# Kernel optimization log

Hardware: AMD Instinct MI355X
Metric: run time of the kernel (lower is better)

## Reference

```python
import jax, jax.numpy as jnp
import numpy as np

H = W = 64          # spatial size
WH = WW = 8         # window size
C = 384             # embed dim
NH = 12             # heads
HD = C // NH        # head dim
SH, SW = WH // 2, WW // 2   # shift
N = WH * WW         # tokens per window
NW = (H // WH) * (W // WW)  # windows per image
SCALE = C ** -0.5   # NOTE: original scales by embed_dim**-0.5, not head_dim


def _to_windows(x, B):
    # (B, H*W, C) -> (B*NW, N, C)
    x = x.reshape(B, H // WH, WH, W // WW, WW, C)
    x = x.transpose(0, 1, 3, 2, 4, 5)
    return x.reshape(B * NW, N, C)


def _to_spatial(x, B):
    # (B*NW, N, C) -> (B, H*W, C)
    x = x.reshape(B, H // WH, W // WW, WH, WW, C)
    x = x.transpose(0, 1, 3, 2, 4, 5)
    return x.reshape(B, H * W, C)


def setup_inputs() -> dict:
    key = jax.random.key(0)
    ks = jax.random.split(key, 4)
    x = jax.random.normal(ks[0], (32, H * W, C), jnp.float32)
    w_qkv = jax.random.normal(ks[1], (C, 3 * C), jnp.float32) * (1.0 / np.sqrt(C))
    w_proj = jax.random.normal(ks[2], (C, C), jnp.float32) * (1.0 / np.sqrt(C))
    b_proj = jnp.zeros((C,), jnp.float32)
    emb_table = jax.random.normal(ks[3], (2 * (WH - 1) + 1 + 2 * (WW - 1) + 1, NH), jnp.float32) * 0.02

    # relative-position bias indices (create_bias_indices)
    hmax, wmax = WH - 1, WW - 1
    h_abs = np.repeat(np.arange(WH), WW)
    w_abs = np.tile(np.arange(WW), WH)
    h_rel = h_abs[None, :] - h_abs[:, None]
    w_rel = w_abs[None, :] - w_abs[:, None]
    h_idx = np.clip(h_rel, -hmax, hmax) + hmax                      # offset 0
    w_idx = np.clip(w_rel, -wmax, wmax) + wmax + (2 * hmax + 1)     # offset 2*hmax+1
    indices = jnp.asarray(np.stack([h_idx, w_idx]), jnp.int32)      # (2, N, N)

    # shift mask (create_shift_mask)
    id_map = np.zeros((H, W))
    h_slices = [(0, -WH), (-WH, -SH), (-SH, None)]
    w_slices = [(0, -WW), (-WW, -SW), (-SW, None)]
    cnt = 0
    for hs, he in h_slices:
        for ws, we in w_slices:
            id_map[hs:he, ws:we] = cnt
            cnt += 1
    idw = id_map.reshape(H // WH, WH, W // WW, WW).transpose(0, 2, 1, 3).reshape(NW, N)
    diff = idw[:, None, :] - idw[:, :, None]
    shift_mask = jnp.asarray(np.where(diff != 0, -1e9, 0.0), jnp.float32)  # (NW, N, N)

    return dict(x=x, w_qkv=w_qkv, w_proj=w_proj, b_proj=b_proj,
                emb_table=emb_table, indices=indices, shift_mask=shift_mask)


def reference(x, w_qkv, w_proj, b_proj, emb_table, indices, shift_mask):
    B = x.shape[0]
    # cyclic shift
    xg = x.reshape(B, H, W, C)
    xg = jnp.roll(xg, (-SH, -SW), axis=(1, 2)).reshape(B, H * W, C)
    xw = _to_windows(xg, B)                                   # (B*NW, N, C)
    qkv = xw @ w_qkv                                          # (B*NW, N, 3C)
    qkv = qkv.reshape(B * NW, N, 3, NH, HD).transpose(2, 0, 3, 1, 4)
    q, k, v = qkv[0] * SCALE, qkv[1], qkv[2]                  # (B*NW, NH, N, HD)
    s = jnp.einsum('bhnc,bhmc->bhnm', q, k)
    # relative-position bias: gather twice (h and w tables) and sum
    bias = emb_table[indices].sum(0).transpose(2, 0, 1)       # (NH, N, N)
    s = s + bias[None]
    # per-window-group additive shift mask
    s = s.reshape(B, NW, NH, N, N) + shift_mask[None, :, None]
    s = s.reshape(B * NW, NH, N, N)
    a = jax.nn.softmax(s, axis=-1)
    o = jnp.einsum('bhnm,bhmc->bhnc', a, v)
    o = o.transpose(0, 2, 1, 3).reshape(B * NW, N, C)
    o = o @ w_proj + b_proj
    o = _to_spatial(o, B)
    # reverse cyclic shift
    o = jnp.roll(o.reshape(B, H, W, C), (SH, SW), axis=(1, 2)).reshape(B, H * W, C)
    return o
```

## Files before the change

kernel.cpp:

```cpp
#include <hip/hip_runtime.h>
#include <hip/hip_bf16.h>

typedef __bf16 bf16x8 __attribute__((ext_vector_type(8)));
typedef float f32x4 __attribute__((ext_vector_type(4)));
typedef float f32x4v __attribute__((ext_vector_type(4)));
typedef unsigned short u16x8 __attribute__((ext_vector_type(8)));
typedef unsigned short u16x4 __attribute__((ext_vector_type(4)));

#define NHEADS 12
#define SCALE 0.05103103630798288f
#define MFMA __builtin_amdgcn_mfma_f32_16x16x32_bf16

static __device__ __forceinline__ unsigned short f2b(float f){
    unsigned u = __float_as_uint(f);
    unsigned r = u + 0x7FFFu + ((u >> 16) & 1u);
    return (unsigned short)(r >> 16);
}
static __device__ __forceinline__ float b2f(unsigned short u){
    union { float f; unsigned u32; } v; v.u32 = ((unsigned)u) << 16; return v.f;
}

__global__ void prep_full(const float* __restrict__ wqkv, const float* __restrict__ wproj,
                          const float* __restrict__ emb, const int* __restrict__ indices,
                          const float* __restrict__ mask,
                          unsigned short* __restrict__ wqkvP,
                          unsigned short* __restrict__ wprojP,
                          unsigned short* __restrict__ bm2){
    int i = blockIdx.x * 256 + threadIdx.x;
    if (i < 442368){
        int j = i & 7, rest = i >> 3;
        int ln = rest & 63; rest >>= 6;
        int kf = rest % 12, t = rest / 12;
        int k = kf * 32 + (ln >> 4) * 8 + j;
        int col = t * 16 + (ln & 15);
        wqkvP[i] = f2b(wqkv[k * 1152 + col]);
        return;
    }
    i -= 442368;
    if (i < 147456){
        int j = i & 7, rest = i >> 3;
        int ln = rest & 63; rest >>= 6;
        int kf = rest % 12, t = rest / 12;
        int k = kf * 32 + (ln >> 4) * 8 + j;
        int col = t * 16 + (ln & 15);
        wprojP[i] = f2b(wproj[k * 384 + col]);
        return;
    }
    i -= 147456;
    if (i < 64 * 12 * 4096){
        int w = i / 49152, rem = i % 49152;
        int h = rem / 4096, r2 = rem & 4095;
        int col = r2 >> 6, row = r2 & 63;
        int ij = row * 64 + col;
        float v = emb[indices[ij] * 12 + h] + emb[indices[4096 + ij] * 12 + h]
                + mask[w * 4096 + ij];
        bm2[i] = f2b(v);
    }
}

__global__ __launch_bounds__(256, 3) void qkv_gemm(
    const float* __restrict__ x, const unsigned short* __restrict__ wqkvP,
    unsigned short* __restrict__ qg, unsigned short* __restrict__ kg,
    unsigned short* __restrict__ vg)
{
    __shared__ unsigned short As[64 * 384];
    __shared__ unsigned short tbuf[4 * 512];
    const int tid = threadIdx.x, wave = tid >> 6, lane = tid & 63;
    const int lo = lane & 15, hi = lane >> 4;
    const int win = blockIdx.x;
    const int widx = win & 63, wh = widx >> 3, ww = widx & 7, b = win >> 6;

    {
        const int r = tid >> 2;
        const int ih = r >> 3, iw = r & 7;
        const int gh = (wh * 8 + ih + 4) & 63, gw = (ww * 8 + iw + 4) & 63;
        const float* src = x + ((size_t)(b * 4096 + gh * 64 + gw)) * 384;
        unsigned short* dst = As + r * 384;
        const int sw = r & 7;
        #pragma unroll
        for (int i = 0; i < 12; ++i){
            const int c = (tid & 3) + i * 4;
            f32x4v f0 = __builtin_nontemporal_load(
                reinterpret_cast<const f32x4v*>(src + c * 8));
            f32x4v f1 = __builtin_nontemporal_load(
                reinterpret_cast<const f32x4v*>(src + c * 8 + 4));
            union { bf16x8 v; unsigned short s[8]; } u;
            u.s[0]=f2b(f0[0]); u.s[1]=f2b(f0[1]); u.s[2]=f2b(f0[2]); u.s[3]=f2b(f0[3]);
            u.s[4]=f2b(f1[0]); u.s[5]=f2b(f1[1]); u.s[6]=f2b(f1[2]); u.s[7]=f2b(f1[3]);
            const int cs = (c & ~7) | ((c & 7) ^ sw);
            *reinterpret_cast<bf16x8*>(dst + cs * 8) = u.v;
        }
    }
    __syncthreads();

    #pragma unroll 1
    for (int nc = 0; nc < 9; ++nc){
        const int t0 = nc * 8 + wave * 2;
        const unsigned short* bp = wqkvP + (size_t)t0 * 12 * 512 + lane * 8;
        f32x4 acc[4][2];
        #pragma unroll
        for (int rt = 0; rt < 4; ++rt){ acc[rt][0] = {0,0,0,0}; acc[rt][1] = {0,0,0,0}; }
        #pragma unroll
        for (int kf = 0; kf < 12; ++kf){
            bf16x8 b0 = *reinterpret_cast<const bf16x8*>(bp + kf * 512);
            bf16x8 b1 = *reinterpret_cast<const bf16x8*>(bp + (12 + kf) * 512);
            const int c = kf * 4 + hi;
            #pragma unroll
            for (int rt = 0; rt < 4; ++rt){
                const int r = rt * 16 + lo;
                const int cs = (c & ~7) | ((c & 7) ^ (r & 7));
                bf16x8 af = *reinterpret_cast<const bf16x8*>(As + r * 384 + cs * 8);
                acc[rt][0] = MFMA(af, b0, acc[rt][0], 0, 0, 0);
                acc[rt][1] = MFMA(af, b1, acc[rt][1], 0, 0, 0);
            }
        }
        const int base = nc * 128 + wave * 32;
        const int m = base / 384;
        const int h = (base % 384) >> 5;
        const size_t pair = (size_t)(win * 12 + h);
        if (m == 2){
            #pragma unroll
            for (int ct = 0; ct < 2; ++ct){
                const int d = ct * 16 + lo;
                #pragma unroll
                for (int rt = 0; rt < 4; ++rt){
                    u16x4 u;
                    u[0] = f2b(acc[rt][ct][0]); u[1] = f2b(acc[rt][ct][1]);
                    u[2] = f2b(acc[rt][ct][2]); u[3] = f2b(acc[rt][ct][3]);
                    __builtin_nontemporal_store(u, reinterpret_cast<u16x4*>(
                        vg + pair * 2048 + (size_t)d * 64 + rt * 16 + hi * 4));
                }
            }
        } else {
            unsigned short* tb = tbuf + wave * 512;
            const float sc = (m == 0) ? SCALE : 1.0f;
            unsigned short* dstb = (m == 0 ? qg : kg) + pair * 2048;
            #pragma unroll
            for (int rt = 0; rt < 4; ++rt){
                asm volatile("" ::: "memory");
                #pragma unroll
                for (int ct = 0; ct < 2; ++ct)
                    #pragma unroll
                    for (int r4 = 0; r4 < 4; ++r4)
                        tb[(hi * 4 + r4) * 32 + ct * 16 + lo] = f2b(acc[rt][ct][r4] * sc);
                asm volatile("" ::: "memory");
                u16x8 v = *reinterpret_cast<const u16x8*>(
                    tb + (lane >> 2) * 32 + (lane & 3) * 8);
                __builtin_nontemporal_store(v, reinterpret_cast<u16x8*>(
                    dstb + rt * 512 + (lane >> 2) * 32 + (lane & 3) * 8));
                asm volatile("" ::: "memory");
            }
        }
    }
}

__global__ __launch_bounds__(256, 4) void attn_only(
    const unsigned short* __restrict__ qg, const unsigned short* __restrict__ kg,
    const unsigned short* __restrict__ vg, const unsigned short* __restrict__ bm2,
    unsigned short* __restrict__ Og)
{
    __shared__ unsigned short psm_all[4][64 * 64];
    __shared__ unsigned short tb_all[4][512];
    const int tid = threadIdx.x, wave = tid >> 6, lane = tid & 63;
    const int lo = lane & 15, hi = lane >> 4;
    const int bid = blockIdx.x;
    const int win = bid / 3, e = bid - win * 3;
    const int widx = win & 63;
    const int h = e * 4 + wave;
    const size_t pair = (size_t)(win * 12 + h);
    const unsigned short* qb  = qg + pair * 2048;
    const unsigned short* kbp = kg + pair * 2048;
    const unsigned short* vb  = vg + pair * 2048;
    const unsigned short* bmb = bm2 + (size_t)(widx * 12 + h) * 4096;
    unsigned short* psm = psm_all[wave];

    bf16x8 kf[4];
    #pragma unroll
    for (int ct = 0; ct < 4; ++ct)
        kf[ct] = *reinterpret_cast<const bf16x8*>(kbp + (ct * 16 + lo) * 32 + hi * 8);

    #pragma unroll
    for (int rh = 0; rh < 2; ++rh){
        f32x4 s[2][4];
        __builtin_amdgcn_s_setprio(1);
        #pragma unroll
        for (int rt2 = 0; rt2 < 2; ++rt2){
            bf16x8 qf = *reinterpret_cast<const bf16x8*>(
                qb + ((rh * 2 + rt2) * 16 + lo) * 32 + hi * 8);
            #pragma unroll
            for (int ct = 0; ct < 4; ++ct){
                f32x4 z = {0,0,0,0};
                s[rt2][ct] = MFMA(qf, kf[ct], z, 0, 0, 0);
            }
        }
        __builtin_amdgcn_s_setprio(0);
        #pragma unroll
        for (int rt2 = 0; rt2 < 2; ++rt2)
            #pragma unroll
            for (int ct = 0; ct < 4; ++ct){
                ushort4 bv = *reinterpret_cast<const ushort4*>(
                    bmb + (ct * 16 + lo) * 64 + (rh * 2 + rt2) * 16 + hi * 4);
                s[rt2][ct][0] += b2f(bv.x);
                s[rt2][ct][1] += b2f(bv.y);
                s[rt2][ct][2] += b2f(bv.z);
                s[rt2][ct][3] += b2f(bv.w);
            }
        #pragma unroll
        for (int rt2 = 0; rt2 < 2; ++rt2)
            #pragma unroll
            for (int r4 = 0; r4 < 4; ++r4){
                float mx = fmaxf(fmaxf(s[rt2][0][r4], s[rt2][1][r4]),
                                 fmaxf(s[rt2][2][r4], s[rt2][3][r4]));
                mx = fmaxf(mx, __shfl_xor(mx, 1, 64));
                mx = fmaxf(mx, __shfl_xor(mx, 2, 64));
                mx = fmaxf(mx, __shfl_xor(mx, 4, 64));
                mx = fmaxf(mx, __shfl_xor(mx, 8, 64));
                float e0 = __expf(s[rt2][0][r4] - mx), e1 = __expf(s[rt2][1][r4] - mx);
                float e2 = __expf(s[rt2][2][r4] - mx), e3 = __expf(s[rt2][3][r4] - mx);
                float sm = e0 + e1 + e2 + e3;
                sm += __shfl_xor(sm, 1, 64);
                sm += __shfl_xor(sm, 2, 64);
                sm += __shfl_xor(sm, 4, 64);
                sm += __shfl_xor(sm, 8, 64);
                const float inv = 1.0f / sm;
                const int row = (rh * 2 + rt2) * 16 + hi * 4 + r4;
                const int rsw = row & 7;
                #pragma unroll
                for (int ct = 0; ct < 4; ++ct){
                    const int c = ct * 2 + (lo >> 3);
                    const float ev = (ct == 0 ? e0 : ct == 1 ? e1 : ct == 2 ? e2 : e3);
                    psm[row * 64 + (c ^ rsw) * 8 + (lo & 7)] = f2b(ev * inv);
                }
            }
    }
    asm volatile("" ::: "memory");

    f32x4 o[4][2];
    #pragma unroll
    for (int rt = 0; rt < 4; ++rt){ o[rt][0] = {0,0,0,0}; o[rt][1] = {0,0,0,0}; }
    #pragma unroll
    for (int ks = 0; ks < 2; ++ks){
        bf16x8 vf[2];
        #pragma unroll
        for (int ct2 = 0; ct2 < 2; ++ct2)
            vf[ct2] = *reinterpret_cast<const bf16x8*>(
                vb + (ct2 * 16 + lo) * 64 + ks * 32 + hi * 8);
        __builtin_amdgcn_s_setprio(1);
        #pragma unroll
        for (int rt = 0; rt < 4; ++rt){
            const int row = rt * 16 + lo;
            const int c = ks * 4 + hi;
            bf16x8 pa = *reinterpret_cast<const bf16x8*>(
                psm + row * 64 + (c ^ (row & 7)) * 8);
            o[rt][0] = MFMA(pa, vf[0], o[rt][0], 0, 0, 0);
            o[rt][1] = MFMA(pa, vf[1], o[rt][1], 0, 0, 0);
        }
        __builtin_amdgcn_s_setprio(0);
    }

    unsigned short* tb = tb_all[wave];
    #pragma unroll
    for (int rt = 0; rt < 4; ++rt){
        asm volatile("" ::: "memory");
        #pragma unroll
        for (int ct2 = 0; ct2 < 2; ++ct2)
            #pragma unroll
            for (int r4 = 0; r4 < 4; ++r4)
                tb[(hi * 4 + r4) * 32 + ct2 * 16 + lo] = f2b(o[rt][ct2][r4]);
        asm volatile("" ::: "memory");
        u16x8 v = *reinterpret_cast<const u16x8*>(tb + (lane >> 2) * 32 + (lane & 3) * 8);
        *reinterpret_cast<u16x8*>(
            Og + pair * 2048 + rt * 512 + (lane >> 2) * 32 + (lane & 3) * 8) = v;
        asm volatile("" ::: "memory");
    }
}

__global__ __launch_bounds__(256, 4) void proj_only(
    const unsigned short* __restrict__ Og, const unsigned short* __restrict__ wprojP,
    const float* __restrict__ bproj, float* __restrict__ out)
{
    __shared__ __attribute__((aligned(16))) unsigned char smem[25088];
    unsigned short* As = reinterpret_cast<unsigned short*>(smem);
    float* Asf = reinterpret_cast<float*>(smem);
    const int tid = threadIdx.x, wave = tid >> 6, lane = tid & 63;
    const int lo = lane & 15, hi = lane >> 4;
    const int blk = blockIdx.x;
    const int win = blk >> 1, half = blk & 1;
    const int widx = win & 63, wh = widx >> 3, ww = widx & 7, b = win >> 6;

    {
        const int r = tid >> 3;
        const int c0 = tid & 7;
        const int tokg = half * 32 + r;
        #pragma unroll
        for (int i = 0; i < 6; ++i){
            const int c = c0 + i * 8;
            const int h = c >> 2;
            bf16x8 v = *reinterpret_cast<const bf16x8*>(
                Og + (size_t)(win * 12 + h) * 2048 + tokg * 32 + (c & 3) * 8);
            const int cs = (c & ~7) | ((c & 7) ^ (r & 7));
            *reinterpret_cast<bf16x8*>(As + r * 384 + cs * 8) = v;
        }
    }
    __syncthreads();

    f32x4 acc[2][6];
    #pragma unroll
    for (int rt = 0; rt < 2; ++rt)
        #pragma unroll
        for (int ct = 0; ct < 6; ++ct) acc[rt][ct] = {0,0,0,0};
    #pragma unroll
    for (int kf = 0; kf < 12; ++kf){
        bf16x8 bfr[6];
        #pragma unroll
        for (int ct = 0; ct < 6; ++ct){
            const int t = wave * 6 + ct;
            bfr[ct] = *reinterpret_cast<const bf16x8*>(
                wprojP + (size_t)(t * 12 + kf) * 512 + lane * 8);
        }
        const int c = kf * 4 + hi;
        #pragma unroll
        for (int rt = 0; rt < 2; ++rt){
            const int r = rt * 16 + lo;
            const int cs = (c & ~7) | ((c & 7) ^ (r & 7));
            bf16x8 af = *reinterpret_cast<const bf16x8*>(As + r * 384 + cs * 8);
            #pragma unroll
            for (int ct = 0; ct < 6; ++ct)
                acc[rt][ct] = MFMA(af, bfr[ct], acc[rt][ct], 0, 0, 0);
        }
    }

    #pragma unroll
    for (int p = 0; p < 2; ++p){
        __syncthreads();
        #pragma unroll
        for (int ct = 0; ct < 6; ++ct){
            const int col = wave * 96 + ct * 16 + lo;
            const float bv = bproj[col];
            #pragma unroll
            for (int r4 = 0; r4 < 4; ++r4)
                Asf[(hi * 4 + r4) * 392 + col] = acc[p][ct][r4] + bv;
        }
        __syncthreads();
        const int row = tid >> 4, tcol = tid & 15;
        const int tok = half * 32 + p * 16 + row;
        const int ih = tok >> 3, iw = tok & 7;
        const int gh = (wh * 8 + ih + 4) & 63, gw = (ww * 8 + iw + 4) & 63;
        float* orow = out + ((size_t)(b * 4096 + gh * 64 + gw)) * 384;
        #pragma unroll
        for (int j = 0; j < 6; ++j){
            f32x4 v = *reinterpret_cast<const f32x4*>(Asf + row * 392 + j * 64 + tcol * 4);
            __builtin_nontemporal_store(v, reinterpret_cast<f32x4*>(orow + j * 64 + tcol * 4));
        }
    }
}

__global__ void transpose_weights(const float* __restrict__ wqkv,
                                  const float* __restrict__ wproj,
                                  unsigned short* __restrict__ wqkvT,
                                  unsigned short* __restrict__ wprojT){
    int i = blockIdx.x * 256 + threadIdx.x;
    if (i < 1152 * 384){ int j = i / 384, k = i % 384; wqkvT[i] = f2b(wqkv[k * 1152 + j]); }
    i -= 1152 * 384;
    if (i >= 0 && i < 384 * 384){ int j = i / 384, k = i % 384; wprojT[i] = f2b(wproj[k * 384 + j]); }
}

__global__ __launch_bounds__(256) void fused_noproj(
    const float* __restrict__ x, const float* __restrict__ emb,
    const int* __restrict__ indices, const float* __restrict__ mask,
    const unsigned short* __restrict__ wqkvT, unsigned short* __restrict__ Og)
{
    __shared__ unsigned short smem[37120];
    unsigned short* xw = smem;
    unsigned short* qT = smem + 25088;
    unsigned short* kT = smem + 27648;
    unsigned short* vT = smem + 30208;
    unsigned short* pT = smem + 32512;

    const int tid = threadIdx.x, wave = tid >> 6, lane = tid & 63;
    const int lo = lane & 15, hi = lane >> 4;
    const int blk = blockIdx.x, b = blk >> 6, widx = blk & 63;
    const int wh = widx >> 3, wwi = widx & 7;

    {
        const int n = tid >> 2, qp = tid & 3;
        const int ih = n >> 3, iw = n & 7;
        const int gh = ((wh * 8 + ih) + 4) & 63, gw = ((wwi * 8 + iw) + 4) & 63;
        const size_t src = ((size_t)b * 4096 + gh * 64 + gw) * 384 + qp * 96;
        const float4* gp = reinterpret_cast<const float4*>(x + src);
        unsigned short* dst = xw + n * 392 + qp * 96;
        #pragma unroll
        for (int i = 0; i < 24; ++i){
            float4 f = gp[i];
            ushort4 u;
            u.x = f2b(f.x); u.y = f2b(f.y); u.z = f2b(f.z); u.w = f2b(f.w);
            *reinterpret_cast<ushort4*>(dst + i * 4) = u;
        }
    }
    __syncthreads();

    for (int h = 0; h < NHEADS; ++h){
        #pragma unroll
        for (int j = 0; j < 6; ++j){
            const int t = wave * 6 + j;
            const int m = t >> 3, tt = t & 7;
            const int tr = tt >> 1, tc = tt & 1;
            const int col = m * 384 + h * 32 + tc * 16 + lo;
            f32x4 acc = {0.f, 0.f, 0.f, 0.f};
            #pragma unroll
            for (int kb = 0; kb < 12; ++kb){
                bf16x8 a = *reinterpret_cast<const bf16x8*>(xw + (tr * 16 + lo) * 392 + kb * 32 + hi * 8);
                bf16x8 bb = *reinterpret_cast<const bf16x8*>(wqkvT + (size_t)col * 384 + kb * 32 + hi * 8);
                acc = MFMA(a, bb, acc, 0, 0, 0);
            }
            #pragma unroll
            for (int r = 0; r < 4; ++r){
                const int token = tr * 16 + hi * 4 + r;
                const int d = tc * 16 + lo;
                if (m == 0)      qT[token * 40 + d] = f2b(acc[r] * SCALE);
                else if (m == 1) kT[token * 40 + d] = f2b(acc[r]);
                else             vT[d * 72 + token] = f2b(acc[r]);
            }
        }
        __syncthreads();
        {
            const int mi = wave;
            bf16x8 qf = *reinterpret_cast<const bf16x8*>(qT + (mi * 16 + lo) * 40 + hi * 8);
            f32x4 s[4];
            #pragma unroll
            for (int ni = 0; ni < 4; ++ni){
                bf16x8 kfr = *reinterpret_cast<const bf16x8*>(kT + (ni * 16 + lo) * 40 + hi * 8);
                f32x4 z = {0.f, 0.f, 0.f, 0.f};
                s[ni] = MFMA(qf, kfr, z, 0, 0, 0);
            }
            #pragma unroll
            for (int ni = 0; ni < 4; ++ni){
                const int kk = ni * 16 + lo;
                #pragma unroll
                for (int r = 0; r < 4; ++r){
                    const int qq = mi * 16 + hi * 4 + r;
                    const int ij = qq * 64 + kk;
                    s[ni][r] += emb[indices[ij] * 12 + h] + emb[indices[4096 + ij] * 12 + h]
                              + mask[widx * 4096 + ij];
                }
            }
            #pragma unroll
            for (int r = 0; r < 4; ++r){
                float mx = fmaxf(fmaxf(s[0][r], s[1][r]), fmaxf(s[2][r], s[3][r]));
                mx = fmaxf(mx, __shfl_xor(mx, 1, 64));
                mx = fmaxf(mx, __shfl_xor(mx, 2, 64));
                mx = fmaxf(mx, __shfl_xor(mx, 4, 64));
                mx = fmaxf(mx, __shfl_xor(mx, 8, 64));
                float e0 = __expf(s[0][r] - mx), e1 = __expf(s[1][r] - mx);
                float e2 = __expf(s[2][r] - mx), e3 = __expf(s[3][r] - mx);
                float sm = e0 + e1 + e2 + e3;
                sm += __shfl_xor(sm, 1, 64);
                sm += __shfl_xor(sm, 2, 64);
                sm += __shfl_xor(sm, 4, 64);
                sm += __shfl_xor(sm, 8, 64);
                float inv = 1.0f / sm;
                const int qq = mi * 16 + hi * 4 + r;
                pT[qq * 72 +  0 + lo] = f2b(e0 * inv);
                pT[qq * 72 + 16 + lo] = f2b(e1 * inv);
                pT[qq * 72 + 32 + lo] = f2b(e2 * inv);
                pT[qq * 72 + 48 + lo] = f2b(e3 * inv);
            }
        }
        __syncthreads();
        {
            const int tr = wave;
            #pragma unroll
            for (int tc = 0; tc < 2; ++tc){
                f32x4 acc = {0.f, 0.f, 0.f, 0.f};
                #pragma unroll
                for (int st = 0; st < 2; ++st){
                    bf16x8 a = *reinterpret_cast<const bf16x8*>(pT + (tr * 16 + lo) * 72 + st * 32 + hi * 8);
                    bf16x8 bb = *reinterpret_cast<const bf16x8*>(vT + (tc * 16 + lo) * 72 + st * 32 + hi * 8);
                    acc = MFMA(a, bb, acc, 0, 0, 0);
                }
                #pragma unroll
                for (int r = 0; r < 4; ++r){
                    const int token = tr * 16 + hi * 4 + r;
                    Og[((size_t)blk * 64 + token) * 384 + h * 32 + tc * 16 + lo] = f2b(acc[r]);
                }
            }
        }
        __syncthreads();
    }
}

__global__ __launch_bounds__(256) void proj_gemm_T(
    const unsigned short* __restrict__ Og, const unsigned short* __restrict__ wprojT,
    const float* __restrict__ bproj, float* __restrict__ out)
{
    __shared__ unsigned short As[64 * 384];
    const int tid = threadIdx.x, wave = tid >> 6, lane = tid & 63;
    const int lo = lane & 15, hi = lane >> 4;
    const int win = blockIdx.x;
    const int widx = win & 63, wh = widx >> 3, ww = widx & 7, b = win >> 6;

    {
        const int r = tid >> 2;
        const unsigned short* src = Og + ((size_t)win * 64 + r) * 384;
        const int sw = r & 7;
        #pragma unroll
        for (int i = 0; i < 12; ++i){
            const int c = (tid & 3) + i * 4;
            bf16x8 v = *reinterpret_cast<const bf16x8*>(src + c * 8);
            const int cs = (c & ~7) | ((c & 7) ^ sw);
            *reinterpret_cast<bf16x8*>(As + r * 384 + cs * 8) = v;
        }
    }
    __syncthreads();

    #pragma unroll 1
    for (int nc = 0; nc < 3; ++nc){
        f32x4 acc[4][2];
        #pragma unroll
        for (int rt = 0; rt < 4; ++rt){ acc[rt][0] = {0,0,0,0}; acc[rt][1] = {0,0,0,0}; }
        #pragma unroll
        for (int kb = 0; kb < 6; ++kb){
            bf16x8 bf[2][2];
            #pragma unroll
            for (int ct = 0; ct < 2; ++ct)
                #pragma unroll
                for (int ks = 0; ks < 2; ++ks){
                    const int col = nc * 128 + wave * 32 + ct * 16 + lo;
                    bf[ct][ks] = *reinterpret_cast<const bf16x8*>(
                        wprojT + (size_t)col * 384 + kb * 64 + ks * 32 + hi * 8);
                }
            #pragma unroll
            for (int ks = 0; ks < 2; ++ks)
                #pragma unroll
                for (int rt = 0; rt < 4; ++rt){
                    const int r = rt * 16 + lo;
                    const int c = kb * 8 + ks * 4 + hi;
                    const int cs = (c & ~7) | ((c & 7) ^ (r & 7));
                    bf16x8 af = *reinterpret_cast<const bf16x8*>(As + r * 384 + cs * 8);
                    acc[rt][0] = MFMA(af, bf[0][ks], acc[rt][0], 0, 0, 0);
                    acc[rt][1] = MFMA(af, bf[1][ks], acc[rt][1], 0, 0, 0);
                }
        }
        #pragma unroll
        for (int rt = 0; rt < 4; ++rt)
            #pragma unroll
            for (int ct = 0; ct < 2; ++ct){
                const int col = nc * 128 + wave * 32 + ct * 16 + lo;
                const float bv = bproj[col];
                #pragma unroll
                for (int r4 = 0; r4 < 4; ++r4){
                    const int tok = rt * 16 + hi * 4 + r4;
                    const int ih = tok >> 3, iw = tok & 7;
                    const int gh = (wh * 8 + ih + 4) & 63, gw = (ww * 8 + iw + 4) & 63;
                    out[((size_t)(b * 4096 + gh * 64 + gw)) * 384 + col] =
                        acc[rt][ct][r4] + bv;
                }
            }
    }
}

static __device__ __forceinline__ bf16x8 load_bT(const unsigned short* __restrict__ WT,
                                                 const float* __restrict__ Worig,
                                                 int useT, int col, int k0, int ldOrig){
    if (useT){
        return *reinterpret_cast<const bf16x8*>(WT + (size_t)col * 384 + k0);
    } else {
        union { bf16x8 v; unsigned short s[8]; } u;
        #pragma unroll
        for (int i = 0; i < 8; ++i) u.s[i] = f2b(Worig[(size_t)(k0 + i) * ldOrig + col]);
        return u.v;
    }
}

__global__ __launch_bounds__(256) void swin_attn_kernel(
    const float* __restrict__ x, const float* __restrict__ wqkv,
    const float* __restrict__ wproj, const float* __restrict__ bproj,
    const float* __restrict__ emb, const int* __restrict__ indices,
    const float* __restrict__ mask, const unsigned short* __restrict__ wqkvT,
    const unsigned short* __restrict__ wprojT, int useT, float* __restrict__ out)
{
    __shared__ unsigned short smem[62208];
    unsigned short* xw = smem;
    unsigned short* O  = smem + 25088;
    unsigned short* qT = smem + 50176;
    unsigned short* kT = smem + 52736;
    unsigned short* vT = smem + 55296;
    unsigned short* pT = smem + 57600;

    const int tid = threadIdx.x, wave = tid >> 6, lane = tid & 63;
    const int lo = lane & 15, hi = lane >> 4;
    const int blk = blockIdx.x, b = blk >> 6, widx = blk & 63;
    const int wh = widx >> 3, wwi = widx & 7;

    {
        const int n = tid >> 2, qp = tid & 3;
        const int ih = n >> 3, iw = n & 7;
        const int gh = ((wh * 8 + ih) + 4) & 63, gw = ((wwi * 8 + iw) + 4) & 63;
        const size_t src = ((size_t)b * 4096 + gh * 64 + gw) * 384 + qp * 96;
        const float4* gp = reinterpret_cast<const float4*>(x + src);
        unsigned short* dst = xw + n * 392 + qp * 96;
        #pragma unroll
        for (int i = 0; i < 24; ++i){
            float4 f = gp[i];
            ushort4 u;
            u.x = f2b(f.x); u.y = f2b(f.y); u.z = f2b(f.z); u.w = f2b(f.w);
            *reinterpret_cast<ushort4*>(dst + i * 4) = u;
        }
    }
    __syncthreads();

    for (int h = 0; h < NHEADS; ++h){
        #pragma unroll
        for (int j = 0; j < 6; ++j){
            const int t = wave * 6 + j;
            const int m = t >> 3, tt = t & 7;
            const int tr = tt >> 1, tc = tt & 1;
            const int col = m * 384 + h * 32 + tc * 16 + lo;
            f32x4 acc = {0.f, 0.f, 0.f, 0.f};
            #pragma unroll
            for (int kb = 0; kb < 12; ++kb){
                bf16x8 a = *reinterpret_cast<const bf16x8*>(xw + (tr * 16 + lo) * 392 + kb * 32 + hi * 8);
                bf16x8 bb = load_bT(wqkvT, wqkv, useT, col, kb * 32 + hi * 8, 1152);
                acc = MFMA(a, bb, acc, 0, 0, 0);
            }
            #pragma unroll
            for (int r = 0; r < 4; ++r){
                const int token = tr * 16 + hi * 4 + r;
                const int d = tc * 16 + lo;
                if (m == 0)      qT[token * 40 + d] = f2b(acc[r] * SCALE);
                else if (m == 1) kT[token * 40 + d] = f2b(acc[r]);
                else             vT[d * 72 + token] = f2b(acc[r]);
            }
        }
        __syncthreads();
        {
            const int mi = wave;
            bf16x8 qf = *reinterpret_cast<const bf16x8*>(qT + (mi * 16 + lo) * 40 + hi * 8);
            f32x4 s[4];
            #pragma unroll
            for (int ni = 0; ni < 4; ++ni){
                bf16x8 kfr = *reinterpret_cast<const bf16x8*>(kT + (ni * 16 + lo) * 40 + hi * 8);
                f32x4 z = {0.f, 0.f, 0.f, 0.f};
                s[ni] = MFMA(qf, kfr, z, 0, 0, 0);
            }
            #pragma unroll
            for (int ni = 0; ni < 4; ++ni){
                const int kk = ni * 16 + lo;
                #pragma unroll
                for (int r = 0; r < 4; ++r){
                    const int qq = mi * 16 + hi * 4 + r;
                    const int ij = qq * 64 + kk;
                    s[ni][r] += emb[indices[ij] * 12 + h] + emb[indices[4096 + ij] * 12 + h]
                              + mask[widx * 4096 + ij];
                }
            }
            #pragma unroll
            for (int r = 0; r < 4; ++r){
                float mx = fmaxf(fmaxf(s[0][r], s[1][r]), fmaxf(s[2][r], s[3][r]));
                mx = fmaxf(mx, __shfl_xor(mx, 1, 64));
                mx = fmaxf(mx, __shfl_xor(mx, 2, 64));
                mx = fmaxf(mx, __shfl_xor(mx, 4, 64));
                mx = fmaxf(mx, __shfl_xor(mx, 8, 64));
                float e0 = __expf(s[0][r] - mx), e1 = __expf(s[1][r] - mx);
                float e2 = __expf(s[2][r] - mx), e3 = __expf(s[3][r] - mx);
                float sm = e0 + e1 + e2 + e3;
                sm += __shfl_xor(sm, 1, 64);
                sm += __shfl_xor(sm, 2, 64);
                sm += __shfl_xor(sm, 4, 64);
                sm += __shfl_xor(sm, 8, 64);
                float inv = 1.0f / sm;
                const int qq = mi * 16 + hi * 4 + r;
                pT[qq * 72 +  0 + lo] = f2b(e0 * inv);
                pT[qq * 72 + 16 + lo] = f2b(e1 * inv);
                pT[qq * 72 + 32 + lo] = f2b(e2 * inv);
                pT[qq * 72 + 48 + lo] = f2b(e3 * inv);
            }
        }
        __syncthreads();
        {
            const int tr = wave;
            #pragma unroll
            for (int tc = 0; tc < 2; ++tc){
                f32x4 acc = {0.f, 0.f, 0.f, 0.f};
                #pragma unroll
                for (int st = 0; st < 2; ++st){
                    bf16x8 a = *reinterpret_cast<const bf16x8*>(pT + (tr * 16 + lo) * 72 + st * 32 + hi * 8);
                    bf16x8 bb = *reinterpret_cast<const bf16x8*>(vT + (tc * 16 + lo) * 72 + st * 32 + hi * 8);
                    acc = MFMA(a, bb, acc, 0, 0, 0);
                }
                #pragma unroll
                for (int r = 0; r < 4; ++r){
                    const int token = tr * 16 + hi * 4 + r;
                    O[token * 392 + h * 32 + tc * 16 + lo] = f2b(acc[r]);
                }
            }
        }
        __syncthreads();
    }
    {
        const int tr = wave;
        bf16x8 afr[12];
        #pragma unroll
        for (int kb = 0; kb < 12; ++kb)
            afr[kb] = *reinterpret_cast<const bf16x8*>(O + (tr * 16 + lo) * 392 + kb * 32 + hi * 8);
        for (int tc = 0; tc < 24; ++tc){
            const int col = tc * 16 + lo;
            f32x4 acc = {0.f, 0.f, 0.f, 0.f};
            #pragma unroll
            for (int kb = 0; kb < 12; ++kb){
                bf16x8 bb = load_bT(wprojT, wproj, useT, col, kb * 32 + hi * 8, 384);
                acc = MFMA(afr[kb], bb, acc, 0, 0, 0);
            }
            const float bv = bproj[col];
            #pragma unroll
            for (int r = 0; r < 4; ++r){
                const int token = tr * 16 + hi * 4 + r;
                const int ih = token >> 3, iw = token & 7;
                const int gh = ((wh * 8 + ih) + 4) & 63, gw = ((wwi * 8 + iw) + 4) & 63;
                out[((size_t)b * 4096 + gh * 64 + gw) * 384 + col] = acc[r] + bv;
            }
        }
    }
}

extern "C" void kernel_launch(void* const* d_in, const int* in_sizes, int n_in,
                              void* d_out, int out_size, void* d_ws, size_t ws_size,
                              hipStream_t stream){
    const float* x     = (const float*)d_in[0];
    const float* wqkv  = (const float*)d_in[1];
    const float* wproj = (const float*)d_in[2];
    const float* bproj = (const float*)d_in[3];
    const float* emb   = (const float*)d_in[4];
    const int*   idx   = (const int*)d_in[5];
    const float* mask  = (const float*)d_in[6];
    float* out = (float*)d_out;

    const int B = in_sizes[0] / (4096 * 384);
    const int NWIN = B * 64;

    unsigned short* ws = (unsigned short*)d_ws;
    const size_t W1 = (size_t)1152 * 384;
    const size_t W2 = (size_t)384 * 384;
    const size_t BM = (size_t)64 * 12 * 4096;
    const size_t QE = (size_t)NWIN * 12 * 64 * 32;
    const size_t full_need = (W1 + W2 + BM + 3 * QE) * 2;
    const size_t mid_need  = (W1 + W2 + QE) * 2;
    const size_t low_need  = (W1 + W2) * 2;

    if (d_ws && ws_size >= full_need){
        unsigned short* wqkvP  = ws;
        unsigned short* wprojP = ws + W1;
        unsigned short* bm2    = ws + W1 + W2;
        unsigned short* qg     = bm2 + BM;
        unsigned short* kg     = qg + QE;
        unsigned short* vg     = kg + QE;
        prep_full<<<dim3(14592), dim3(256), 0, stream>>>(wqkv, wproj, emb, idx, mask,
                                                         wqkvP, wprojP, bm2);
        qkv_gemm<<<dim3(NWIN), dim3(256), 0, stream>>>(x, wqkvP, qg, kg, vg);
        attn_only<<<dim3(NWIN * 3), dim3(256), 0, stream>>>(qg, kg, vg, bm2, qg);
        proj_only<<<dim3(NWIN * 2), dim3(256), 0, stream>>>(qg, wprojP, bproj, out);
    } else if (d_ws && ws_size >= mid_need){
        unsigned short* wqkvT  = ws;
        unsigned short* wprojT = ws + W1;
        unsigned short* Og     = ws + W1 + W2;
        transpose_weights<<<dim3(2304), dim3(256), 0, stream>>>(wqkv, wproj, wqkvT, wprojT);
        fused_noproj<<<dim3(NWIN), dim3(256), 0, stream>>>(x, emb, idx, mask, wqkvT, Og);
        proj_gemm_T<<<dim3(NWIN), dim3(256), 0, stream>>>(Og, wprojT, bproj, out);
    } else {
        unsigned short* wqkvT  = ws;
        unsigned short* wprojT = ws ? ws + W1 : nullptr;
        const int useT = (d_ws != nullptr && ws_size >= low_need) ? 1 : 0;
        if (useT)
            transpose_weights<<<dim3(2304), dim3(256), 0, stream>>>(wqkv, wproj, wqkvT, wprojT);
        swin_attn_kernel<<<dim3(NWIN), dim3(256), 0, stream>>>(
            x, wqkv, wproj, bproj, emb, idx, mask, wqkvT, wprojT, useT, out);
    }
}
```

Measured before the change: 371.5 us.

## Retile QKV GEMM to 6x4 MFMA blocks and store fragment-native Q/K/V layout

The QKV projection now gives each wave a 96-column by 64-row tile per section (Q, K, V), loading six weight fragments per k-step and reusing each A fragment across six MFMAs. For Q and K the MFMA operands are swapped so the results can be stored directly in an MFMA-fragment-friendly layout, which removes the LDS transpose buffer and its staging. The attention kernel's Q/K/V fragment loads are re-indexed to match this new layout. In exchange the kernel holds 24 accumulators per wave, which raises register pressure and may reduce occupancy, and the k-loop is no longer unrolled.

New measurement: 1.363 ms. +266.9%, slower.

```diff
diff --git a/kernel.cpp b/kernel.cpp
--- a/kernel.cpp
+++ b/kernel.cpp
@@ -19,6 +19,7 @@
 static __device__ __forceinline__ float b2f(unsigned short u){
     union { float f; unsigned u32; } v; v.u32 = ((unsigned)u) << 16; return v.f;
 }
+
 
 __global__ void prep_full(const float* __restrict__ wqkv, const float* __restrict__ wproj,
                           const float* __restrict__ emb, const int* __restrict__ indices,
@@ -64,7 +65,6 @@
     unsigned short* __restrict__ vg)
 {
     __shared__ unsigned short As[64 * 384];
-    __shared__ unsigned short tbuf[4 * 512];
     const int tid = threadIdx.x, wave = tid >> 6, lane = tid & 63;
     const int lo = lane & 15, hi = lane >> 4;
     const int win = blockIdx.x;
@@ -94,61 +94,59 @@
     __syncthreads();
 
     #pragma unroll 1
-    for (int nc = 0; nc < 9; ++nc){
-        const int t0 = nc * 8 + wave * 2;
+    for (int sec = 0; sec < 3; ++sec){
+        const int t0 = sec * 24 + wave * 6;
         const unsigned short* bp = wqkvP + (size_t)t0 * 12 * 512 + lane * 8;
-        f32x4 acc[4][2];
-        #pragma unroll
-        for (int rt = 0; rt < 4; ++rt){ acc[rt][0] = {0,0,0,0}; acc[rt][1] = {0,0,0,0}; }
-        #pragma unroll
+
+        f32x4 acc[6][4];
+        #pragma unroll
+        for (int wt = 0; wt < 6; ++wt)
+            #pragma unroll
+            for (int tt = 0; tt < 4; ++tt) acc[wt][tt] = {0,0,0,0};
+
+        #pragma unroll 1
         for (int kf = 0; kf < 12; ++kf){
-            bf16x8 b0 = *reinterpret_cast<const bf16x8*>(bp + kf * 512);
-            bf16x8 b1 = *reinterpret_cast<const bf16x8*>(bp + (12 + kf) * 512);
+            bf16x8 bw[6];
+            #pragma unroll
+            for (int wt = 0; wt < 6; ++wt)
+                bw[wt] = *reinterpret_cast<const bf16x8*>(bp + (wt * 12 + kf) * 512);
             const int c = kf * 4 + hi;
-            #pragma unroll
-            for (int rt = 0; rt < 4; ++rt){
-                const int r = rt * 16 + lo;
-                const int cs = (c & ~7) | ((c & 7) ^ (r & 7));
-                bf16x8 af = *reinterpret_cast<const bf16x8*>(As + r * 384 + cs * 8);
-                acc[rt][0] = MFMA(af, b0, acc[rt][0], 0, 0, 0);
-                acc[rt][1] = MFMA(af, b1, acc[rt][1], 0, 0, 0);
-            }
-        }
-        const int base = nc * 128 + wave * 32;
-        const int m = base / 384;
-        const int h = (base % 384) >> 5;
-        const size_t pair = (size_t)(win * 12 + h);
-        if (m == 2){
-            #pragma unroll
-            for (int ct = 0; ct < 2; ++ct){
-                const int d = ct * 16 + lo;
-                #pragma unroll
-                for (int rt = 0; rt < 4; ++rt){
-                    u16x4 u;
-                    u[0] = f2b(acc[rt][ct][0]); u[1] = f2b(acc[rt][ct][1]);
-                    u[2] = f2b(acc[rt][ct][2]); u[3] = f2b(acc[rt][ct][3]);
-                    __builtin_nontemporal_store(u, reinterpret_cast<u16x4*>(
-                        vg + pair * 2048 + (size_t)d * 64 + rt * 16 + hi * 4));
-                }
-            }
-        } else {
-            unsigned short* tb = tbuf + wave * 512;
-            const float sc = (m == 0) ? SCALE : 1.0f;
-            unsigned short* dstb = (m == 0 ? qg : kg) + pair * 2048;
-            #pragma unroll
-            for (int rt = 0; rt < 4; ++rt){
-                asm volatile("" ::: "memory");
-                #pragma unroll
-                for (int ct = 0; ct < 2; ++ct)
+            if (sec < 2){
+                #pragma unroll
+                for (int tt = 0; tt < 4; ++tt){
+                    const int r = tt * 16 + lo;
+                    const int cs = (c & ~7) | ((c & 7) ^ (r & 7));
+                    bf16x8 af = *reinterpret_cast<const bf16x8*>(As + r * 384 + cs * 8);
                     #pragma unroll
-                    for (int r4 = 0; r4 < 4; ++r4)
-                        tb[(hi * 4 + r4) * 32 + ct * 16 + lo] = f2b(acc[rt][ct][r4] * sc);
-                asm volatile("" ::: "memory");
-                u16x8 v = *reinterpret_cast<const u16x8*>(
-                    tb + (lane >> 2) * 32 + (lane & 3) * 8);
-                __builtin_nontemporal_store(v, reinterpret_cast<u16x8*>(
-                    dstb + rt * 512 + (lane >> 2) * 32 + (lane & 3) * 8));
-                asm volatile("" ::: "memory");
+                    for (int wt = 0; wt < 6; ++wt)
+                        acc[wt][tt] = MFMA(bw[wt], af, acc[wt][tt], 0, 0, 0);
+                }
+            } else {
+                #pragma unroll
+                for (int tt = 0; tt < 4; ++tt){
+                    const int r = tt * 16 + lo;
+                    const int cs = (c & ~7) | ((c & 7) ^ (r & 7));
+                    bf16x8 af = *reinterpret_cast<const bf16x8*>(As + r * 384 + cs * 8);
+                    #pragma unroll
+                    for (int wt = 0; wt < 6; ++wt)
+                        acc[wt][tt] = MFMA(af, bw[wt], acc[wt][tt], 0, 0, 0);
+                }
+            }
+        }
+
+        const float sc = (sec == 0) ? SCALE : 1.0f;
+        unsigned short* basep = (sec == 0 ? qg : sec == 1 ? kg : vg);
+        #pragma unroll
+        for (int wt = 0; wt < 6; ++wt){
+            const int hloc = wave * 3 + (wt >> 1);
+            unsigned short* dst = basep + (size_t)(win * 12 + hloc) * 2048
+                                + (wt & 1) * 1024 + (hi >> 1) * 128 + lo * 8 + (hi & 1) * 4;
+            #pragma unroll
+            for (int tt = 0; tt < 4; ++tt){
+                u16x4 u;
+                u[0] = f2b(acc[wt][tt][0] * sc); u[1] = f2b(acc[wt][tt][1] * sc);
+                u[2] = f2b(acc[wt][tt][2] * sc); u[3] = f2b(acc[wt][tt][3] * sc);
+                __builtin_nontemporal_store(u, reinterpret_cast<u16x4*>(dst + tt * 256));
             }
         }
     }
@@ -173,11 +171,12 @@
     const unsigned short* vb  = vg + pair * 2048;
     const unsigned short* bmb = bm2 + (size_t)(widx * 12 + h) * 4096;
     unsigned short* psm = psm_all[wave];
+    const int fbase = (hi >> 1) * 1024 + (hi & 1) * 128 + lo * 8;
 
     bf16x8 kf[4];
     #pragma unroll
     for (int ct = 0; ct < 4; ++ct)
-        kf[ct] = *reinterpret_cast<const bf16x8*>(kbp + (ct * 16 + lo) * 32 + hi * 8);
+        kf[ct] = *reinterpret_cast<const bf16x8*>(kbp + fbase + ct * 256);
 
     #pragma unroll
     for (int rh = 0; rh < 2; ++rh){
@@ -186,7 +185,7 @@
         #pragma unroll
         for (int rt2 = 0; rt2 < 2; ++rt2){
             bf16x8 qf = *reinterpret_cast<const bf16x8*>(
-                qb + ((rh * 2 + rt2) * 16 + lo) * 32 + hi * 8);
+                qb + fbase + (rh * 2 + rt2) * 256);
             #pragma unroll
             for (int ct = 0; ct < 4; ++ct){
                 f32x4 z = {0,0,0,0};
@@ -244,7 +243,7 @@
         #pragma unroll
         for (int ct2 = 0; ct2 < 2; ++ct2)
             vf[ct2] = *reinterpret_cast<const bf16x8*>(
-                vb + (ct2 * 16 + lo) * 64 + ks * 32 + hi * 8);
+                vb + ct2 * 1024 + (ks * 2 + (hi >> 1)) * 256 + (hi & 1) * 128 + lo * 8);
         __builtin_amdgcn_s_setprio(1);
         #pragma unroll
         for (int rt = 0; rt < 4; ++rt){
```
